# Optimization experiments

Hardware: AMD Instinct MI355X
Metric: run time of the kernel (lower is better)

The kernel has to match this reference:

```python
import jax, jax.numpy as jnp
import numpy as np

B, H, S, DK, DV = 2, 16, 2048, 64, 64


def setup_inputs() -> dict:
    key = jax.random.key(0)
    kq, kk, kv = jax.random.split(key, 3)
    queries = jax.random.normal(kq, (B, H, S, DK), dtype=jnp.float32)
    keys = jax.random.normal(kk, (B, H, S, DK), dtype=jnp.float32)
    values = jax.random.normal(kv, (B, H, S, DV), dtype=jnp.float32)
    # causal boolean mask, broadcastable over batch and heads
    mask = jnp.tril(jnp.ones((S, S), dtype=bool))[None, None, :, :]
    return {"queries": queries, "keys": keys, "values": values, "d_k": DK, "mask": mask}


def reference(queries, keys, values, d_k, mask):
    scale = 1.0 / jnp.sqrt(jnp.float32(d_k))
    # scores: [B, H, S, S]
    scores = jnp.einsum("bhqd,bhkd->bhqk", queries, keys) * scale
    mask_f = mask.astype(jnp.float32)
    scores = scores + (-1e9) * (1.0 - mask_f)
    weights = jax.nn.softmax(scores, axis=-1)
    # second mask step from the original: min(|mask|, |weights|)
    weights = jnp.minimum(jnp.abs(mask_f), jnp.abs(weights))
    return jnp.einsum("bhqk,bhkd->bhqd", weights, values)
```

## Files before the change

kernel.cpp:

```cpp
#include <hip/hip_runtime.h>
#include <hip/hip_bf16.h>

#define B_ 2
#define H_ 16
#define S_ 2048
#define D_ 64

typedef __attribute__((ext_vector_type(8))) short bf16x8;
typedef __attribute__((ext_vector_type(8))) unsigned short u16x8;
typedef __attribute__((ext_vector_type(4))) unsigned int u32x4;
typedef __attribute__((ext_vector_type(4))) float f32x4;
typedef unsigned short ushort_t;

#define SCALE 0.18033688011112042f

__device__ __forceinline__ unsigned short f2bf(float x) {
  unsigned int u = __builtin_bit_cast(unsigned int, x);
  unsigned int r = (u + 0x7FFFu + ((u >> 16) & 1u)) >> 16;
  return (unsigned short)r;
}

__device__ __forceinline__ unsigned int cvt_pk_bf16(float lo, float hi) {
  unsigned int r;
  asm("v_cvt_pk_bf16_f32 %0, %1, %2" : "=v"(r) : "v"(lo), "v"(hi));
  return r;
}

__device__ __forceinline__ int sigma_row(int rl) {
  return (rl & 0x23) | ((rl & 0x0C) << 1) | ((rl & 0x10) >> 2);
}

#define GLL16(gp, lp)                                                          \
  __builtin_amdgcn_global_load_lds(                                            \
      (const __attribute__((address_space(1))) unsigned int*)(gp),             \
      (__attribute__((address_space(3))) unsigned int*)(lp), 16, 0, 0)

__global__ void prepack(const float* __restrict__ Kf, const float* __restrict__ Vf,
                        ushort_t* __restrict__ Kg, ushort_t* __restrict__ Vtg) {
  const int blk = blockIdx.x;
  const int tid = threadIdx.x;
  const int bh = blk >> 5, t = blk & 31;
  const float* srcK = Kf + ((size_t)bh * S_ + (size_t)t * 64) * D_;
  const float* srcV = Vf + ((size_t)bh * S_ + (size_t)t * 64) * D_;
  ushort_t* dK = Kg + (size_t)blk * 4096;
  ushort_t* dV = Vtg + (size_t)blk * 4096;
  for (int is = 0; is < 2; ++is) {
    const int e = is * 2048 + tid * 8;
    {
      const int rl = e >> 6, pos = (e >> 3) & 7, ch = pos ^ (rl & 7);
      const float* sp = srcK + sigma_row(rl) * 64 + ch * 8;
      float4 a = *(const float4*)sp;
      float4 b = *(const float4*)(sp + 4);
      u16x8 w;
      w[0] = f2bf(a.x); w[1] = f2bf(a.y); w[2] = f2bf(a.z); w[3] = f2bf(a.w);
      w[4] = f2bf(b.x); w[5] = f2bf(b.y); w[6] = f2bf(b.z); w[7] = f2bf(b.w);
      *(u16x8*)(dK + e) = w;
    }
    {
      const int d0 = e >> 6, pos = (e >> 3) & 7, ch = pos ^ (d0 & 7);
      u16x8 w;
      for (int i = 0; i < 8; ++i) w[i] = f2bf(srcV[(size_t)(ch * 8 + i) * 64 + d0]);
      *(u16x8*)(dV + e) = w;
    }
  }
}

template <int PRE>
__launch_bounds__(256, 4)
__global__ void attn6(const float* __restrict__ Qf, const float* __restrict__ Kf,
                      const float* __restrict__ Vf, const ushort_t* __restrict__ Kg,
                      const ushort_t* __restrict__ Vtg, float* __restrict__ O) {
  const int bh = blockIdx.x;
  const int qt = 31 - blockIdx.y;
  const int tid = threadIdx.x;
  const int wave = tid >> 6, lane = tid & 63;
  const int col = lane & 15, g = lane >> 4;

  __shared__ __align__(16) ushort_t Kl[2][64][64];
  __shared__ __align__(16) ushort_t Vt[2][64][64];

  float* Oh = O + (size_t)bh * S_ * D_;

  const int qrow = qt * 64 + wave * 16 + col;
  bf16x8 qf[2];
  {
    const float* Qh = Qf + (size_t)bh * S_ * D_;
    for (int kk = 0; kk < 2; ++kk) {
      const float* p = Qh + (size_t)qrow * 64 + kk * 32 + g * 8;
      float4 a = *(const float4*)p;
      float4 b = *(const float4*)(p + 4);
      float v[8] = {a.x, a.y, a.z, a.w, b.x, b.y, b.z, b.w};
      bf16x8 w;
      for (int i = 0; i < 8; ++i) w[i] = (short)f2bf(v[i] * SCALE);
      qf[kk] = w;
    }
  }

  f32x4 acc[4] = {};
  float m_ = -INFINITY, l_ = 0.0f;

  const int ch0 = (g ^ (col & 7)) << 3;
  const int ch1 = ((4 | g) ^ (col & 7)) << 3;

  auto STAGE = [&](int t, int b) {
    if (PRE) {
      const ushort_t* kg = Kg + ((size_t)(bh * 32 + t)) * 4096;
      const ushort_t* vg = Vtg + ((size_t)(bh * 32 + t)) * 4096;
      GLL16(kg + tid * 8,        &Kl[b][0][0] + tid * 8);
      GLL16(kg + 2048 + tid * 8, &Kl[b][0][0] + 2048 + tid * 8);
      GLL16(vg + tid * 8,        &Vt[b][0][0] + tid * 8);
      GLL16(vg + 2048 + tid * 8, &Vt[b][0][0] + 2048 + tid * 8);
    } else {
      const float* Kh = Kf + (size_t)bh * S_ * D_;
      const float* Vh = Vf + (size_t)bh * S_ * D_;
      {
        const int rl = tid >> 2;
        const int c0 = (tid & 3) << 4;
        const float* src = Kh + ((size_t)(t * 64 + sigma_row(rl))) * 64 + c0;
        for (int jj = 0; jj < 2; ++jj) {
          float4 x = *(const float4*)(src + jj * 8);
          float4 y = *(const float4*)(src + jj * 8 + 4);
          u16x8 w;
          w[0] = f2bf(x.x); w[1] = f2bf(x.y); w[2] = f2bf(x.z); w[3] = f2bf(x.w);
          w[4] = f2bf(y.x); w[5] = f2bf(y.y); w[6] = f2bf(y.z); w[7] = f2bf(y.w);
          const int ch = (c0 >> 3) + jj;
          *(u16x8*)&Kl[b][rl][(ch ^ (rl & 7)) << 3] = w;
        }
      }
      {
        const int c = tid & 63;
        const int r0 = (tid >> 6) << 4;
        const float* src = Vh + ((size_t)(t * 64 + r0)) * 64 + c;
        for (int jj = 0; jj < 2; ++jj) {
          u16x8 w;
          for (int i = 0; i < 8; ++i) w[i] = f2bf(src[(size_t)(jj * 8 + i) * 64]);
          const int ch = (r0 >> 3) + jj;
          *(u16x8*)&Vt[b][c][(ch ^ (c & 7)) << 3] = w;
        }
      }
    }
  };

  auto COMPUTE = [&](int b, bool diag) {
    f32x4 s[4] = {{0,0,0,0},{0,0,0,0},{0,0,0,0},{0,0,0,0}};
    __builtin_amdgcn_s_setprio(1);
    for (int nt = 0; nt < 4; ++nt) {
      const ushort_t* row = &Kl[b][nt * 16 + col][0];
      const bf16x8 kf0 = *(const bf16x8*)(row + ch0);
      const bf16x8 kf1 = *(const bf16x8*)(row + ch1);
      s[nt] = __builtin_amdgcn_mfma_f32_16x16x32_bf16(kf0, qf[0], s[nt], 0, 0, 0);
      s[nt] = __builtin_amdgcn_mfma_f32_16x16x32_bf16(kf1, qf[1], s[nt], 0, 0, 0);
    }
    __builtin_amdgcn_s_setprio(0);
    if (diag) {
      const int qloc = wave * 16 + col;
      #pragma unroll
      for (int nt = 0; nt < 4; ++nt) {
        const int tau_base = 32 * (nt >> 1) + 4 * (nt & 1) + 8 * g;
        #pragma unroll
        for (int r = 0; r < 4; ++r)
          if (tau_base + r > qloc) s[nt][r] = -INFINITY;
      }
    }
    float pm = fmaxf(fmaxf(fmaxf(s[0][0], s[0][1]), fmaxf(s[0][2], s[0][3])),
                     fmaxf(fmaxf(s[1][0], s[1][1]), fmaxf(s[1][2], s[1][3])));
    pm = fmaxf(pm, fmaxf(fmaxf(fmaxf(s[2][0], s[2][1]), fmaxf(s[2][2], s[2][3])),
                         fmaxf(fmaxf(s[3][0], s[3][1]), fmaxf(s[3][2], s[3][3]))));
    pm = fmaxf(pm, __shfl_xor(pm, 16));
    pm = fmaxf(pm, __shfl_xor(pm, 32));
    float fac = 1.0f;
    if (!__all(pm - m_ <= 8.0f)) {
      const float mn = fmaxf(m_, pm);
      fac = exp2f(m_ - mn);
      m_ = mn;
      for (int nt = 0; nt < 4; ++nt) acc[nt] *= fac;
    }
    float sum = 0.0f;
    for (int nt = 0; nt < 4; ++nt)
      for (int r = 0; r < 4; ++r) {
        const float p = exp2f(s[nt][r] - m_);
        s[nt][r] = p;
        sum += p;
      }
    sum += __shfl_xor(sum, 16);
    sum += __shfl_xor(sum, 32);
    l_ = l_ * fac + sum;
    u32x4 t0, t1;
    t0[0] = cvt_pk_bf16(s[0][0], s[0][1]); t0[1] = cvt_pk_bf16(s[0][2], s[0][3]);
    t0[2] = cvt_pk_bf16(s[1][0], s[1][1]); t0[3] = cvt_pk_bf16(s[1][2], s[1][3]);
    t1[0] = cvt_pk_bf16(s[2][0], s[2][1]); t1[1] = cvt_pk_bf16(s[2][2], s[2][3]);
    t1[2] = cvt_pk_bf16(s[3][0], s[3][1]); t1[3] = cvt_pk_bf16(s[3][2], s[3][3]);
    const bf16x8 pf0 = __builtin_bit_cast(bf16x8, t0);
    const bf16x8 pf1 = __builtin_bit_cast(bf16x8, t1);
    __builtin_amdgcn_s_setprio(1);
    for (int nt = 0; nt < 4; ++nt) {
      const ushort_t* row = &Vt[b][nt * 16 + col][0];
      const bf16x8 vf0 = *(const bf16x8*)(row + ch0);
      const bf16x8 vf1 = *(const bf16x8*)(row + ch1);
      acc[nt] = __builtin_amdgcn_mfma_f32_16x16x32_bf16(vf0, pf0, acc[nt], 0, 0, 0);
      acc[nt] = __builtin_amdgcn_mfma_f32_16x16x32_bf16(vf1, pf1, acc[nt], 0, 0, 0);
    }
    __builtin_amdgcn_s_setprio(0);
  };

  int cur = 0;
  STAGE(0, 0);
  __syncthreads();
  for (int t = 0; t <= qt; ++t) {
    if (t < qt) STAGE(t + 1, cur ^ 1);
    COMPUTE(cur, t == qt);
    __syncthreads();
    cur ^= 1;
  }

  const float inv = 1.0f / l_;
  float* dst = Oh + (size_t)qrow * 64;
  for (int nt = 0; nt < 4; ++nt) {
    f32x4 v = acc[nt];
    v *= inv;
    *(f32x4*)(dst + nt * 16 + 4 * g) = v;
  }
}

extern "C" void kernel_launch(void* const* d_in, const int* in_sizes, int n_in,
                              void* d_out, int out_size, void* d_ws, size_t ws_size,
                              hipStream_t stream) {
  const float* Q = (const float*)d_in[0];
  const float* K = (const float*)d_in[1];
  const float* V = (const float*)d_in[2];
  float* O = (float*)d_out;
  const size_t NE = (size_t)B_ * H_ * S_ * D_;
  if (ws_size >= 2 * NE * sizeof(ushort_t)) {
    ushort_t* kg = (ushort_t*)d_ws;
    prepack<<<1024, 256, 0, stream>>>(K, V, kg, kg + NE);
    attn6<1><<<dim3(32, 32), 256, 0, stream>>>(Q, K, V, kg, kg + NE, O);
  } else {
    attn6<0><<<dim3(32, 32), 256, 0, stream>>>(Q, K, V, nullptr, nullptr, O);
  }
}
```

Baseline: 58.37 us.

## Software-pipeline QK^T one tile ahead with triple-buffered K in LDS

```diff
diff --git a/kernel.cpp b/kernel.cpp
--- a/kernel.cpp
+++ b/kernel.cpp
@@ -24,6 +24,10 @@
   unsigned int r;
   asm("v_cvt_pk_bf16_f32 %0, %1, %2" : "=v"(r) : "v"(lo), "v"(hi));
   return r;
+}
+
+__device__ __forceinline__ float fmax3(float a, float b, float c) {
+  return fmaxf(fmaxf(a, b), c);
 }
 
 __device__ __forceinline__ int sigma_row(int rl) {
@@ -67,7 +71,7 @@
 
 template <int PRE>
 __launch_bounds__(256, 4)
-__global__ void attn6(const float* __restrict__ Qf, const float* __restrict__ Kf,
+__global__ void attn7(const float* __restrict__ Qf, const float* __restrict__ Kf,
                       const float* __restrict__ Vf, const ushort_t* __restrict__ Kg,
                       const ushort_t* __restrict__ Vtg, float* __restrict__ O) {
   const int bh = blockIdx.x;
@@ -76,7 +80,7 @@
   const int wave = tid >> 6, lane = tid & 63;
   const int col = lane & 15, g = lane >> 4;
 
-  __shared__ __align__(16) ushort_t Kl[2][64][64];
+  __shared__ __align__(16) ushort_t Kl[3][64][64];
   __shared__ __align__(16) ushort_t Vt[2][64][64];
 
   float* Oh = O + (size_t)bh * S_ * D_;
@@ -102,56 +106,67 @@
   const int ch0 = (g ^ (col & 7)) << 3;
   const int ch1 = ((4 | g) ^ (col & 7)) << 3;
 
-  auto STAGE = [&](int t, int b) {
+  auto STAGE_K = [&](int t, int kb) {
     if (PRE) {
       const ushort_t* kg = Kg + ((size_t)(bh * 32 + t)) * 4096;
-      const ushort_t* vg = Vtg + ((size_t)(bh * 32 + t)) * 4096;
-      GLL16(kg + tid * 8,        &Kl[b][0][0] + tid * 8);
-      GLL16(kg + 2048 + tid * 8, &Kl[b][0][0] + 2048 + tid * 8);
-      GLL16(vg + tid * 8,        &Vt[b][0][0] + tid * 8);
-      GLL16(vg + 2048 + tid * 8, &Vt[b][0][0] + 2048 + tid * 8);
+      GLL16(kg + tid * 8,        &Kl[kb][0][0] + tid * 8);
+      GLL16(kg + 2048 + tid * 8, &Kl[kb][0][0] + 2048 + tid * 8);
     } else {
       const float* Kh = Kf + (size_t)bh * S_ * D_;
+      const int rl = tid >> 2;
+      const int c0 = (tid & 3) << 4;
+      const float* src = Kh + ((size_t)(t * 64 + sigma_row(rl))) * 64 + c0;
+      for (int jj = 0; jj < 2; ++jj) {
+        float4 x = *(const float4*)(src + jj * 8);
+        float4 y = *(const float4*)(src + jj * 8 + 4);
+        u16x8 w;
+        w[0] = f2bf(x.x); w[1] = f2bf(x.y); w[2] = f2bf(x.z); w[3] = f2bf(x.w);
+        w[4] = f2bf(y.x); w[5] = f2bf(y.y); w[6] = f2bf(y.z); w[7] = f2bf(y.w);
+        const int ch = (c0 >> 3) + jj;
+        *(u16x8*)&Kl[kb][rl][(ch ^ (rl & 7)) << 3] = w;
+      }
+    }
+  };
+  auto STAGE_V = [&](int t, int vb) {
+    if (PRE) {
+      const ushort_t* vg = Vtg + ((size_t)(bh * 32 + t)) * 4096;
+      GLL16(vg + tid * 8,        &Vt[vb][0][0] + tid * 8);
+      GLL16(vg + 2048 + tid * 8, &Vt[vb][0][0] + 2048 + tid * 8);
+    } else {
       const float* Vh = Vf + (size_t)bh * S_ * D_;
-      {
-        const int rl = tid >> 2;
-        const int c0 = (tid & 3) << 4;
-        const float* src = Kh + ((size_t)(t * 64 + sigma_row(rl))) * 64 + c0;
-        for (int jj = 0; jj < 2; ++jj) {
-          float4 x = *(const float4*)(src + jj * 8);
-          float4 y = *(const float4*)(src + jj * 8 + 4);
-          u16x8 w;
-          w[0] = f2bf(x.x); w[1] = f2bf(x.y); w[2] = f2bf(x.z); w[3] = f2bf(x.w);
-          w[4] = f2bf(y.x); w[5] = f2bf(y.y); w[6] = f2bf(y.z); w[7] = f2bf(y.w);
-          const int ch = (c0 >> 3) + jj;
-          *(u16x8*)&Kl[b][rl][(ch ^ (rl & 7)) << 3] = w;
-        }
+      const int c = tid & 63;
+      const int r0 = (tid >> 6) << 4;
+      const float* src = Vh + ((size_t)(t * 64 + r0)) * 64 + c;
+      for (int jj = 0; jj < 2; ++jj) {
+        u16x8 w;
+        for (int i = 0; i < 8; ++i) w[i] = f2bf(src[(size_t)(jj * 8 + i) * 64]);
+        const int ch = (r0 >> 3) + jj;
+        *(u16x8*)&Vt[vb][c][(ch ^ (c & 7)) << 3] = w;
       }
-      {
-        const int c = tid & 63;
-        const int r0 = (tid >> 6) << 4;
-        const float* src = Vh + ((size_t)(t * 64 + r0)) * 64 + c;
-        for (int jj = 0; jj < 2; ++jj) {
-          u16x8 w;
-          for (int i = 0; i < 8; ++i) w[i] = f2bf(src[(size_t)(jj * 8 + i) * 64]);
-          const int ch = (r0 >> 3) + jj;
-          *(u16x8*)&Vt[b][c][(ch ^ (c & 7)) << 3] = w;
-        }
-      }
-    }
-  };
-
-  auto COMPUTE = [&](int b, bool diag) {
-    f32x4 s[4] = {{0,0,0,0},{0,0,0,0},{0,0,0,0},{0,0,0,0}};
+    }
+  };
+
+  bf16x8 kreg[8];
+  auto QK_LOAD = [&](int kb) {
+    #pragma unroll
+    for (int nt = 0; nt < 4; ++nt) {
+      const ushort_t* row = &Kl[kb][nt * 16 + col][0];
+      kreg[2 * nt]     = *(const bf16x8*)(row + ch0);
+      kreg[2 * nt + 1] = *(const bf16x8*)(row + ch1);
+    }
+  };
+  auto QK_MMA = [&](f32x4 (&sn)[4]) {
     __builtin_amdgcn_s_setprio(1);
+    #pragma unroll
     for (int nt = 0; nt < 4; ++nt) {
-      const ushort_t* row = &Kl[b][nt * 16 + col][0];
-      const bf16x8 kf0 = *(const bf16x8*)(row + ch0);
-      const bf16x8 kf1 = *(const bf16x8*)(row + ch1);
-      s[nt] = __builtin_amdgcn_mfma_f32_16x16x32_bf16(kf0, qf[0], s[nt], 0, 0, 0);
-      s[nt] = __builtin_amdgcn_mfma_f32_16x16x32_bf16(kf1, qf[1], s[nt], 0, 0, 0);
+      f32x4 z = {0.f, 0.f, 0.f, 0.f};
+      z = __builtin_amdgcn_mfma_f32_16x16x32_bf16(kreg[2 * nt], qf[0], z, 0, 0, 0);
+      sn[nt] = __builtin_amdgcn_mfma_f32_16x16x32_bf16(kreg[2 * nt + 1], qf[1], z, 0, 0, 0);
     }
     __builtin_amdgcn_s_setprio(0);
+  };
+
+  auto SM = [&](f32x4 (&s)[4], bool diag, bf16x8& pf0, bf16x8& pf1) {
     if (diag) {
       const int qloc = wave * 16 + col;
       #pragma unroll
@@ -162,10 +177,12 @@
           if (tau_base + r > qloc) s[nt][r] = -INFINITY;
       }
     }
-    float pm = fmaxf(fmaxf(fmaxf(s[0][0], s[0][1]), fmaxf(s[0][2], s[0][3])),
-                     fmaxf(fmaxf(s[1][0], s[1][1]), fmaxf(s[1][2], s[1][3])));
-    pm = fmaxf(pm, fmaxf(fmaxf(fmaxf(s[2][0], s[2][1]), fmaxf(s[2][2], s[2][3])),
-                         fmaxf(fmaxf(s[3][0], s[3][1]), fmaxf(s[3][2], s[3][3]))));
+    float a0 = fmax3(s[0][0], s[0][1], s[0][2]);
+    float a1 = fmax3(s[0][3], s[1][0], s[1][1]);
+    float a2 = fmax3(s[1][2], s[1][3], s[2][0]);
+    float a3 = fmax3(s[2][1], s[2][2], s[2][3]);
+    float a4 = fmax3(s[3][0], s[3][1], s[3][2]);
+    float pm = fmax3(fmax3(a0, a1, s[3][3]), fmax3(a2, a3, a4), -INFINITY);
     pm = fmaxf(pm, __shfl_xor(pm, 16));
     pm = fmaxf(pm, __shfl_xor(pm, 32));
     float fac = 1.0f;
@@ -173,28 +190,32 @@
       const float mn = fmaxf(m_, pm);
       fac = exp2f(m_ - mn);
       m_ = mn;
+      #pragma unroll
       for (int nt = 0; nt < 4; ++nt) acc[nt] *= fac;
     }
-    float sum = 0.0f;
+    #pragma unroll
     for (int nt = 0; nt < 4; ++nt)
-      for (int r = 0; r < 4; ++r) {
-        const float p = exp2f(s[nt][r] - m_);
-        s[nt][r] = p;
-        sum += p;
-      }
-    sum += __shfl_xor(sum, 16);
-    sum += __shfl_xor(sum, 32);
-    l_ = l_ * fac + sum;
+      #pragma unroll
+      for (int r = 0; r < 4; ++r) s[nt][r] = exp2f(s[nt][r] - m_);
+    float b0 = (s[0][0] + s[0][1]) + (s[0][2] + s[0][3]);
+    float b1 = (s[1][0] + s[1][1]) + (s[1][2] + s[1][3]);
+    float b2 = (s[2][0] + s[2][1]) + (s[2][2] + s[2][3]);
+    float b3 = (s[3][0] + s[3][1]) + (s[3][2] + s[3][3]);
+    l_ = l_ * fac + ((b0 + b1) + (b2 + b3));
     u32x4 t0, t1;
     t0[0] = cvt_pk_bf16(s[0][0], s[0][1]); t0[1] = cvt_pk_bf16(s[0][2], s[0][3]);
     t0[2] = cvt_pk_bf16(s[1][0], s[1][1]); t0[3] = cvt_pk_bf16(s[1][2], s[1][3]);
     t1[0] = cvt_pk_bf16(s[2][0], s[2][1]); t1[1] = cvt_pk_bf16(s[2][2], s[2][3]);
     t1[2] = cvt_pk_bf16(s[3][0], s[3][1]); t1[3] = cvt_pk_bf16(s[3][2], s[3][3]);
-    const bf16x8 pf0 = __builtin_bit_cast(bf16x8, t0);
-    const bf16x8 pf1 = __builtin_bit_cast(bf16x8, t1);
+    pf0 = __builtin_bit_cast(bf16x8, t0);
+    pf1 = __builtin_bit_cast(bf16x8, t1);
+  };
+
+  auto PV = [&](int vb, bf16x8 pf0, bf16x8 pf1) {
     __builtin_amdgcn_s_setprio(1);
+    #pragma unroll
     for (int nt = 0; nt < 4; ++nt) {
-      const ushort_t* row = &Vt[b][nt * 16 + col][0];
+      const ushort_t* row = &Vt[vb][nt * 16 + col][0];
       const bf16x8 vf0 = *(const bf16x8*)(row + ch0);
       const bf16x8 vf1 = *(const bf16x8*)(row + ch1);
       acc[nt] = __builtin_amdgcn_mfma_f32_16x16x32_bf16(vf0, pf0, acc[nt], 0, 0, 0);
@@ -203,18 +224,38 @@
     __builtin_amdgcn_s_setprio(0);
   };
 
-  int cur = 0;
-  STAGE(0, 0);
+  auto BODY = [&](int t, f32x4 (&cur)[4], f32x4 (&nxt)[4]) {
+    const bool haveN = (t + 1 <= qt);
+    if (t + 2 <= qt) STAGE_K(t + 2, (t + 2) % 3);
+    if (haveN) STAGE_V(t + 1, (t + 1) & 1);
+    if (haveN) QK_LOAD((t + 1) % 3);
+    bf16x8 pf0, pf1;
+    SM(cur, t == qt, pf0, pf1);
+    if (haveN) QK_MMA(nxt);
+    PV(t & 1, pf0, pf1);
+    __syncthreads();
+  };
+
+  STAGE_K(0, 0);
+  STAGE_V(0, 0);
+  if (qt >= 1) STAGE_K(1, 1);
   __syncthreads();
-  for (int t = 0; t <= qt; ++t) {
-    if (t < qt) STAGE(t + 1, cur ^ 1);
-    COMPUTE(cur, t == qt);
-    __syncthreads();
-    cur ^= 1;
-  }
-
-  const float inv = 1.0f / l_;
+  f32x4 sA[4], sB[4];
+  QK_LOAD(0);
+  QK_MMA(sA);
+
+  int t = 0;
+  while (true) {
+    BODY(t, sA, sB); if (++t > qt) break;
+    BODY(t, sB, sA); if (++t > qt) break;
+  }
+
+  float lsum = l_;
+  lsum += __shfl_xor(lsum, 16);
+  lsum += __shfl_xor(lsum, 32);
+  const float inv = 1.0f / lsum;
   float* dst = Oh + (size_t)qrow * 64;
+  #pragma unroll
   for (int nt = 0; nt < 4; ++nt) {
     f32x4 v = acc[nt];
     v *= inv;
@@ -233,8 +274,8 @@
   if (ws_size >= 2 * NE * sizeof(ushort_t)) {
     ushort_t* kg = (ushort_t*)d_ws;
     prepack<<<1024, 256, 0, stream>>>(K, V, kg, kg + NE);
-    attn6<1><<<dim3(32, 32), 256, 0, stream>>>(Q, K, V, kg, kg + NE, O);
+    attn7<1><<<dim3(32, 32), 256, 0, stream>>>(Q, K, V, kg, kg + NE, O);
   } else {
-    attn6<0><<<dim3(32, 32), 256, 0, stream>>>(Q, K, V, nullptr, nullptr, O);
-  }
-}
+    attn7<0><<<dim3(32, 32), 256, 0, stream>>>(Q, K, V, nullptr, nullptr, O);
+  }
+}
```

After: 59.34 us. No clear change (+1.7%).

## Split long causal query tiles across two KV chunks and merge partials

Applied to the files above, without the earlier changes.

```diff
diff --git a/kernel.cpp b/kernel.cpp
--- a/kernel.cpp
+++ b/kernel.cpp
@@ -24,6 +24,16 @@
   unsigned int r;
   asm("v_cvt_pk_bf16_f32 %0, %1, %2" : "=v"(r) : "v"(lo), "v"(hi));
   return r;
+}
+
+__device__ __forceinline__ float fast_exp2(float x) {
+  float r;
+  asm("v_exp_f32 %0, %1" : "=v"(r) : "v"(x));
+  return r;
+}
+
+__device__ __forceinline__ float fmax3(float a, float b, float c) {
+  return fmaxf(fmaxf(a, b), c);
 }
 
 __device__ __forceinline__ int sigma_row(int rl) {
@@ -65,21 +75,27 @@
   }
 }
 
-template <int PRE>
-__launch_bounds__(256, 4)
-__global__ void attn6(const float* __restrict__ Qf, const float* __restrict__ Kf,
-                      const float* __restrict__ Vf, const ushort_t* __restrict__ Kg,
-                      const ushort_t* __restrict__ Vtg, float* __restrict__ O) {
+__launch_bounds__(256, 5)
+__global__ void attn_split(const float* __restrict__ Qf, const ushort_t* __restrict__ Kg,
+                           const ushort_t* __restrict__ Vtg, float* __restrict__ O,
+                           float* __restrict__ PO, float* __restrict__ ML) {
   const int bh = blockIdx.x;
-  const int qt = 31 - blockIdx.y;
+  const int y = blockIdx.y;
+  int qt, c;
+  if (y == 0) { qt = 15; c = 0; }
+  else if (y <= 16) { qt = 15 + y; c = 0; }
+  else if (y == 17) { qt = 31; c = 1; }
+  else { const int p = y - 18, k = 15 - (p >> 1);
+         if (p & 1) { qt = k + 15; c = 1; } else { qt = k - 1; c = 0; } }
+  const int t0 = c << 4;
+  const int t1 = (qt < t0 + 15) ? qt : (t0 + 15);
+
   const int tid = threadIdx.x;
   const int wave = tid >> 6, lane = tid & 63;
   const int col = lane & 15, g = lane >> 4;
 
   __shared__ __align__(16) ushort_t Kl[2][64][64];
   __shared__ __align__(16) ushort_t Vt[2][64][64];
-
-  float* Oh = O + (size_t)bh * S_ * D_;
 
   const int qrow = qt * 64 + wave * 16 + col;
   bf16x8 qf[2];
@@ -102,6 +118,176 @@
   const int ch0 = (g ^ (col & 7)) << 3;
   const int ch1 = ((4 | g) ^ (col & 7)) << 3;
 
+  auto STAGE = [&](int t, int b) {
+    const ushort_t* kg = Kg + ((size_t)(bh * 32 + t)) * 4096;
+    const ushort_t* vg = Vtg + ((size_t)(bh * 32 + t)) * 4096;
+    GLL16(kg + tid * 8,        &Kl[b][0][0] + tid * 8);
+    GLL16(kg + 2048 + tid * 8, &Kl[b][0][0] + 2048 + tid * 8);
+    GLL16(vg + tid * 8,        &Vt[b][0][0] + tid * 8);
+    GLL16(vg + 2048 + tid * 8, &Vt[b][0][0] + 2048 + tid * 8);
+  };
+
+  auto COMPUTE = [&](int b, bool diag) {
+    f32x4 s[4] = {{0,0,0,0},{0,0,0,0},{0,0,0,0},{0,0,0,0}};
+    __builtin_amdgcn_s_setprio(1);
+    #pragma unroll
+    for (int nt = 0; nt < 4; ++nt) {
+      const ushort_t* row = &Kl[b][nt * 16 + col][0];
+      const bf16x8 kf0 = *(const bf16x8*)(row + ch0);
+      const bf16x8 kf1 = *(const bf16x8*)(row + ch1);
+      s[nt] = __builtin_amdgcn_mfma_f32_16x16x32_bf16(kf0, qf[0], s[nt], 0, 0, 0);
+      s[nt] = __builtin_amdgcn_mfma_f32_16x16x32_bf16(kf1, qf[1], s[nt], 0, 0, 0);
+    }
+    __builtin_amdgcn_s_setprio(0);
+    if (diag) {
+      const int qloc = wave * 16 + col;
+      #pragma unroll
+      for (int nt = 0; nt < 4; ++nt) {
+        const int tau_base = 32 * (nt >> 1) + 4 * (nt & 1) + 8 * g;
+        #pragma unroll
+        for (int r = 0; r < 4; ++r)
+          if (tau_base + r > qloc) s[nt][r] = -INFINITY;
+      }
+    }
+    float a0 = fmax3(s[0][0], s[0][1], s[0][2]);
+    float a1 = fmax3(s[0][3], s[1][0], s[1][1]);
+    float a2 = fmax3(s[1][2], s[1][3], s[2][0]);
+    float a3 = fmax3(s[2][1], s[2][2], s[2][3]);
+    float a4 = fmax3(s[3][0], s[3][1], s[3][2]);
+    float pm = fmax3(fmax3(a0, a1, s[3][3]), fmax3(a2, a3, a4), -INFINITY);
+    pm = fmaxf(pm, __shfl_xor(pm, 16));
+    pm = fmaxf(pm, __shfl_xor(pm, 32));
+    float fac = 1.0f;
+    if (!__all(pm - m_ <= 8.0f)) {
+      const float mn = fmaxf(m_, pm);
+      fac = fast_exp2(m_ - mn);
+      m_ = mn;
+      #pragma unroll
+      for (int nt = 0; nt < 4; ++nt) acc[nt] *= fac;
+    }
+    #pragma unroll
+    for (int nt = 0; nt < 4; ++nt)
+      #pragma unroll
+      for (int r = 0; r < 4; ++r) s[nt][r] = fast_exp2(s[nt][r] - m_);
+    float b0 = (s[0][0] + s[0][1]) + (s[0][2] + s[0][3]);
+    float b1 = (s[1][0] + s[1][1]) + (s[1][2] + s[1][3]);
+    float b2 = (s[2][0] + s[2][1]) + (s[2][2] + s[2][3]);
+    float b3 = (s[3][0] + s[3][1]) + (s[3][2] + s[3][3]);
+    l_ = l_ * fac + ((b0 + b1) + (b2 + b3));
+    u32x4 w0, w1;
+    w0[0] = cvt_pk_bf16(s[0][0], s[0][1]); w0[1] = cvt_pk_bf16(s[0][2], s[0][3]);
+    w0[2] = cvt_pk_bf16(s[1][0], s[1][1]); w0[3] = cvt_pk_bf16(s[1][2], s[1][3]);
+    w1[0] = cvt_pk_bf16(s[2][0], s[2][1]); w1[1] = cvt_pk_bf16(s[2][2], s[2][3]);
+    w1[2] = cvt_pk_bf16(s[3][0], s[3][1]); w1[3] = cvt_pk_bf16(s[3][2], s[3][3]);
+    const bf16x8 pf0 = __builtin_bit_cast(bf16x8, w0);
+    const bf16x8 pf1 = __builtin_bit_cast(bf16x8, w1);
+    __builtin_amdgcn_s_setprio(1);
+    #pragma unroll
+    for (int nt = 0; nt < 4; ++nt) {
+      const ushort_t* row = &Vt[b][nt * 16 + col][0];
+      const bf16x8 vf0 = *(const bf16x8*)(row + ch0);
+      const bf16x8 vf1 = *(const bf16x8*)(row + ch1);
+      acc[nt] = __builtin_amdgcn_mfma_f32_16x16x32_bf16(vf0, pf0, acc[nt], 0, 0, 0);
+      acc[nt] = __builtin_amdgcn_mfma_f32_16x16x32_bf16(vf1, pf1, acc[nt], 0, 0, 0);
+    }
+    __builtin_amdgcn_s_setprio(0);
+  };
+
+  int cur = 0;
+  STAGE(t0, 0);
+  __syncthreads();
+  for (int t = t0; t <= t1; ++t) {
+    if (t < t1) STAGE(t + 1, cur ^ 1);
+    COMPUTE(cur, t == qt);
+    __syncthreads();
+    cur ^= 1;
+  }
+
+  float lsum = l_;
+  lsum += __shfl_xor(lsum, 16);
+  lsum += __shfl_xor(lsum, 32);
+  const int rowloc = wave * 16 + col;
+  if (qt <= 15) {
+    const float inv = 1.0f / lsum;
+    float* dst = O + (size_t)bh * S_ * D_ + (size_t)qrow * 64;
+    #pragma unroll
+    for (int nt = 0; nt < 4; ++nt) {
+      f32x4 v = acc[nt];
+      v *= inv;
+      *(f32x4*)(dst + nt * 16 + 4 * g) = v;
+    }
+  } else {
+    float* po = PO + (size_t)((((bh << 4) + (qt - 16)) << 1) + c) * 4096;
+    #pragma unroll
+    for (int nt = 0; nt < 4; ++nt)
+      *(f32x4*)(po + rowloc * 64 + nt * 16 + 4 * g) = acc[nt];
+    if (g == 0) {
+      float* ml = ML + (size_t)((((bh << 4) + (qt - 16)) << 1) + c) * 128 + rowloc * 2;
+      ml[0] = m_;
+      ml[1] = lsum;
+    }
+  }
+}
+
+__global__ void merge_partials(const float* __restrict__ PO, const float* __restrict__ ML,
+                               float* __restrict__ O) {
+  const int bh = blockIdx.x;
+  const int q16 = blockIdx.y;
+  const int tid = threadIdx.x;
+  const int r = tid >> 2, d0 = (tid & 3) << 4;
+  const size_t base = (size_t)((bh << 4) + q16) << 1;
+  const float* ml0 = ML + base * 128 + r * 2;
+  const float* ml1 = ML + (base + 1) * 128 + r * 2;
+  const float m0 = ml0[0], l0 = ml0[1], m1 = ml1[0], l1 = ml1[1];
+  const float M = fmaxf(m0, m1);
+  const float w0 = fast_exp2(m0 - M), w1 = fast_exp2(m1 - M);
+  const float inv = 1.0f / (w0 * l0 + w1 * l1);
+  const float a = w0 * inv, b = w1 * inv;
+  const float* p0 = PO + base * 4096 + r * 64 + d0;
+  const float* p1 = PO + (base + 1) * 4096 + r * 64 + d0;
+  float* out = O + ((size_t)bh * S_ + (size_t)(16 + q16) * 64 + r) * 64 + d0;
+  #pragma unroll
+  for (int j = 0; j < 4; ++j) {
+    float4 x = *(const float4*)(p0 + 4 * j);
+    float4 y = *(const float4*)(p1 + 4 * j);
+    float4 o;
+    o.x = a * x.x + b * y.x; o.y = a * x.y + b * y.y;
+    o.z = a * x.z + b * y.z; o.w = a * x.w + b * y.w;
+    *(float4*)(out + 4 * j) = o;
+  }
+}
+
+template <int PRE>
+__launch_bounds__(256, 4)
+__global__ void attn6(const float* __restrict__ Qf, const float* __restrict__ Kf,
+                      const float* __restrict__ Vf, const ushort_t* __restrict__ Kg,
+                      const ushort_t* __restrict__ Vtg, float* __restrict__ O) {
+  const int bh = blockIdx.x;
+  const int qt = 31 - blockIdx.y;
+  const int tid = threadIdx.x;
+  const int wave = tid >> 6, lane = tid & 63;
+  const int col = lane & 15, g = lane >> 4;
+  __shared__ __align__(16) ushort_t Kl[2][64][64];
+  __shared__ __align__(16) ushort_t Vt[2][64][64];
+  float* Oh = O + (size_t)bh * S_ * D_;
+  const int qrow = qt * 64 + wave * 16 + col;
+  bf16x8 qf[2];
+  {
+    const float* Qh = Qf + (size_t)bh * S_ * D_;
+    for (int kk = 0; kk < 2; ++kk) {
+      const float* p = Qh + (size_t)qrow * 64 + kk * 32 + g * 8;
+      float4 a = *(const float4*)p;
+      float4 b = *(const float4*)(p + 4);
+      float v[8] = {a.x, a.y, a.z, a.w, b.x, b.y, b.z, b.w};
+      bf16x8 w;
+      for (int i = 0; i < 8; ++i) w[i] = (short)f2bf(v[i] * SCALE);
+      qf[kk] = w;
+    }
+  }
+  f32x4 acc[4] = {};
+  float m_ = -INFINITY, l_ = 0.0f;
+  const int ch0 = (g ^ (col & 7)) << 3;
+  const int ch1 = ((4 | g) ^ (col & 7)) << 3;
   auto STAGE = [&](int t, int b) {
     if (PRE) {
       const ushort_t* kg = Kg + ((size_t)(bh * 32 + t)) * 4096;
@@ -140,7 +326,6 @@
       }
     }
   };
-
   auto COMPUTE = [&](int b, bool diag) {
     f32x4 s[4] = {{0,0,0,0},{0,0,0,0},{0,0,0,0},{0,0,0,0}};
     __builtin_amdgcn_s_setprio(1);
@@ -154,10 +339,8 @@
     __builtin_amdgcn_s_setprio(0);
     if (diag) {
       const int qloc = wave * 16 + col;
-      #pragma unroll
       for (int nt = 0; nt < 4; ++nt) {
         const int tau_base = 32 * (nt >> 1) + 4 * (nt & 1) + 8 * g;
-        #pragma unroll
         for (int r = 0; r < 4; ++r)
           if (tau_base + r > qloc) s[nt][r] = -INFINITY;
       }
@@ -171,19 +354,17 @@
     float fac = 1.0f;
     if (!__all(pm - m_ <= 8.0f)) {
       const float mn = fmaxf(m_, pm);
-      fac = exp2f(m_ - mn);
+      fac = fast_exp2(m_ - mn);
       m_ = mn;
       for (int nt = 0; nt < 4; ++nt) acc[nt] *= fac;
     }
     float sum = 0.0f;
     for (int nt = 0; nt < 4; ++nt)
       for (int r = 0; r < 4; ++r) {
-        const float p = exp2f(s[nt][r] - m_);
+        const float p = fast_exp2(s[nt][r] - m_);
         s[nt][r] = p;
         sum += p;
       }
-    sum += __shfl_xor(sum, 16);
-    sum += __shfl_xor(sum, 32);
     l_ = l_ * fac + sum;
     u32x4 t0, t1;
     t0[0] = cvt_pk_bf16(s[0][0], s[0][1]); t0[1] = cvt_pk_bf16(s[0][2], s[0][3]);
@@ -202,7 +383,6 @@
     }
     __builtin_amdgcn_s_setprio(0);
   };
-
   int cur = 0;
   STAGE(0, 0);
   __syncthreads();
@@ -212,8 +392,10 @@
     __syncthreads();
     cur ^= 1;
   }
-
-  const float inv = 1.0f / l_;
+  float lsum = l_;
+  lsum += __shfl_xor(lsum, 16);
+  lsum += __shfl_xor(lsum, 32);
+  const float inv = 1.0f / lsum;
   float* dst = Oh + (size_t)qrow * 64;
   for (int nt = 0; nt < 4; ++nt) {
     f32x4 v = acc[nt];
@@ -230,7 +412,18 @@
   const float* V = (const float*)d_in[2];
   float* O = (float*)d_out;
   const size_t NE = (size_t)B_ * H_ * S_ * D_;
-  if (ws_size >= 2 * NE * sizeof(ushort_t)) {
+  const size_t needK = 2 * NE * sizeof(ushort_t);
+  const size_t PO_elems = 32ull * 16 * 2 * 4096;
+  const size_t ML_elems = 32ull * 16 * 2 * 128;
+  const size_t needSplit = needK + (PO_elems + ML_elems) * sizeof(float);
+  if (ws_size >= needSplit) {
+    ushort_t* kg = (ushort_t*)d_ws;
+    float* PO = (float*)((char*)d_ws + needK);
+    float* ML = PO + PO_elems;
+    prepack<<<1024, 256, 0, stream>>>(K, V, kg, kg + NE);
+    attn_split<<<dim3(32, 48), 256, 0, stream>>>(Q, kg, kg + NE, O, PO, ML);
+    merge_partials<<<dim3(32, 16), 256, 0, stream>>>(PO, ML, O);
+  } else if (ws_size >= needK) {
     ushort_t* kg = (ushort_t*)d_ws;
     prepack<<<1024, 256, 0, stream>>>(K, V, kg, kg + NE);
     attn6<1><<<dim3(32, 32), 256, 0, stream>>>(Q, K, V, kg, kg + NE, O);
```

Result: faster. 55.95 us (-4.1%).
